# Performance work log

Measured on AMD Instinct MI355X. Metric: run time of the kernel, lower is better.

Reference implementation:

```python
import jax, jax.numpy as jnp
import numpy as np

B = 2097152          # number of query points (e.g. one per pixel of a ~1448^2 image)
N_CTRL = 62          # N_ctrl_pts from __init__
GRID = N_CTRL + 2    # control grid size = 64
MASK_B = 1           # maskBoundary
A = -0.75            # PyTorch bicubic convolution coefficient


def _cubic_weights(t):
    # Weights of the Keys cubic kernel (a=-0.75) for taps at offsets (-1,0,1,2).
    # t in [0,1) is the fractional coordinate. Shapes: t [b] -> [b,4].
    s = 1.0 - t
    w0 = A * t * s * s                      # cc2(t+1)
    w1 = (A + 2.0) * t**3 - (A + 3.0) * t**2 + 1.0   # cc1(t)
    w2 = (A + 2.0) * s**3 - (A + 3.0) * s**2 + 1.0   # cc1(1-t)
    w3 = A * s * t * t                      # cc2(2-t)
    return jnp.stack([w0, w1, w2, w3], axis=-1)


def _reflect(idx, size):
    # PyTorch reflection padding with align_corners=True: reflect about 0 and size-1.
    period = 2 * (size - 1)
    idx = jnp.abs(idx) % period
    return jnp.where(idx >= size, period - idx, idx)


def _bicubic_sample(img, coordinate):
    # img: [c, H, W] (same for every query); coordinate: [b, 2] as (y, x) in [-1,1].
    # Equivalent to: affine_grid(theta, size=(b,c,1,1), align_corners=True) +
    # grid_sample(mode='bicubic', padding_mode='reflection', align_corners=True)
    # where theta = [[1/H, 0, x], [0, 1/H, y]] -> single sample at (x-1/H, y-1/H).
    c, H, W = img.shape
    crop = 1.0 / H
    gx = coordinate[:, 1] - crop   # grid x indexes width
    gy = coordinate[:, 0] - crop   # grid y indexes height
    ix = (gx + 1.0) * 0.5 * (W - 1)   # unnormalize, align_corners=True
    iy = (gy + 1.0) * 0.5 * (H - 1)
    ix0 = jnp.floor(ix)
    iy0 = jnp.floor(iy)
    tx = ix - ix0                      # fractional parts (differentiable wrt coords)
    ty = iy - iy0
    offs = jnp.arange(-1, 3, dtype=jnp.int32)
    xs = jnp.clip(_reflect(ix0.astype(jnp.int32)[:, None] + offs, W), 0, W - 1)  # [b,4]
    ys = jnp.clip(_reflect(iy0.astype(jnp.int32)[:, None] + offs, H), 0, H - 1)  # [b,4]
    wx = _cubic_weights(tx)  # [b,4]
    wy = _cubic_weights(ty)  # [b,4]
    # gather 4x4 neighborhoods: vals[c,b,i,j] = img[c, ys[b,i], xs[b,j]]
    vals = img[:, ys[:, :, None], xs[:, None, :]]  # [c, b, 4, 4]
    return jnp.einsum('cbij,bi,bj->bc', vals, wy, wx)  # [b, c]


def _forward(coordinate, depl_ctr_pts, mask):
    img = depl_ctr_pts * mask          # masked control-point displacement field [2,H,W]
    return _bicubic_sample(img, coordinate)  # [b, 2] (torch.squeeze of [b,2,1,1])


def setup_inputs() -> dict:
    key = jax.random.key(0)
    k1, k2 = jax.random.split(key)
    max_ampl = 1.0 / (N_CTRL - 1)
    depl = (jax.random.uniform(k1, (2, GRID, GRID), jnp.float32) - 0.5) * 2.0 * max_ampl
    border = jnp.zeros((GRID,), bool).at[:MASK_B].set(True).at[-MASK_B:].set(True)
    bm = border[:, None] | border[None, :]
    mask = jnp.where(bm[None, :, :], 0.0, jnp.ones((2, GRID, GRID), jnp.float32))
    depl = depl * mask  # __init__ zeros the boundary ring of the stored param too
    coordinate = jax.random.uniform(k2, (B, 2), jnp.float32, minval=-1.0, maxval=1.0)
    return {"coordinate": coordinate, "depl_ctr_pts": depl, "mask": mask}


def reference(coordinate, depl_ctr_pts, mask):
    return _forward(coordinate, depl_ctr_pts, mask)
```

## Files before the change

### kernel.cpp

```cpp
#include <hip/hip_runtime.h>
#include <hip/hip_fp16.h>

#define TPB 256
#define MAXGRID 2048

#define PW 68

__device__ __forceinline__ void cubic_w(float t, float w[4]) {
    float s = 1.0f - t;
    float t2 = t * t;
    float s2 = s * s;
    w[0] = -0.75f * t * s2;
    w[1] = 1.25f * (t2 * t) - 2.25f * t2 + 1.0f;
    w[2] = 1.25f * (s2 * s) - 2.25f * s2 + 1.0f;
    w[3] = -0.75f * s * t2;
}

__global__ __launch_bounds__(TPB, 8) void deformation_field_kernel(
        const float4* __restrict__ coord4,
        const float4* __restrict__ depl4,
        const float4* __restrict__ mask4,
        float4* __restrict__ out4,
        int n_pairs)
{
    __shared__ __half2 img[PW * PW];

    for (int i = threadIdx.x; i < 1024; i += TPB) {
        float4 d0 = depl4[i];
        float4 m0 = mask4[i];
        float4 d1 = depl4[1024 + i];
        float4 m1 = mask4[1024 + i];
        int o = i * 4;
        int r = o >> 6;
        int c = o & 63;
        int pb = (r + 2) * PW + (c + 2);
        img[pb + 0] = __floats2half2_rn(d0.x * m0.x, d1.x * m1.x);
        img[pb + 1] = __floats2half2_rn(d0.y * m0.y, d1.y * m1.y);
        img[pb + 2] = __floats2half2_rn(d0.z * m0.z, d1.z * m1.z);
        img[pb + 3] = __floats2half2_rn(d0.w * m0.w, d1.w * m1.w);
    }
    __syncthreads();

    {
        int t = threadIdx.x;
        int r = 2 + (t & 63);
        int j = t >> 6;
        int sel = j & 1, half = j >> 1;
        int dc = half ? (66 + sel) : sel;
        int sc = half ? (64 - sel) : (4 - sel);
        img[r * PW + dc] = img[r * PW + sc];
    }
    __syncthreads();

    if (threadIdx.x < PW) {
        int c = threadIdx.x;
        img[0 * PW + c]  = img[4 * PW + c];
        img[1 * PW + c]  = img[3 * PW + c];
        img[66 * PW + c] = img[64 * PW + c];
        img[67 * PW + c] = img[63 * PW + c];
    }
    __syncthreads();

    const int stride = gridDim.x * TPB;
    int p = blockIdx.x * TPB + threadIdx.x;
    if (p >= n_pairs) return;

    float4 c = coord4[p];
    for (;;) {
        int pn = p + stride;
        bool has = (pn < n_pairs);
        float4 cn;
        if (has) cn = coord4[pn];

        float res[4];
        #pragma unroll
        for (int q = 0; q < 2; ++q) {
            float cyv = q ? c.z : c.x;
            float cxv = q ? c.w : c.y;
            float ix = (cxv + 0.984375f) * 31.5f;
            float iy = (cyv + 0.984375f) * 31.5f;
            float fx = floorf(ix);
            float fy = floorf(iy);
            float tx = ix - fx;
            float ty = iy - fy;
            int jx = (int)fx;
            int jy = (int)fy;

            float wx[4], wy[4];
            cubic_w(tx, wx);
            cubic_w(ty, wy);

            int base = (jy + 1) * PW + (jx + 1);

            float a0 = 0.0f, a1 = 0.0f;
            #pragma unroll
            for (int i = 0; i < 4; ++i) {
                int rb = base + i * PW;
                __half2 t0 = img[rb + 0];
                __half2 t1 = img[rb + 1];
                __half2 t2 = img[rb + 2];
                __half2 t3 = img[rb + 3];
                float r0 = wx[0] * __low2float(t0);
                float r1 = wx[0] * __high2float(t0);
                r0 = fmaf(wx[1], __low2float(t1), r0);
                r1 = fmaf(wx[1], __high2float(t1), r1);
                r0 = fmaf(wx[2], __low2float(t2), r0);
                r1 = fmaf(wx[2], __high2float(t2), r1);
                r0 = fmaf(wx[3], __low2float(t3), r0);
                r1 = fmaf(wx[3], __high2float(t3), r1);
                a0 = fmaf(wy[i], r0, a0);
                a1 = fmaf(wy[i], r1, a1);
            }
            res[2 * q + 0] = a0;
            res[2 * q + 1] = a1;
        }
        out4[p] = make_float4(res[0], res[1], res[2], res[3]);

        if (!has) break;
        p = pn;
        c = cn;
    }
}

extern "C" void kernel_launch(void* const* d_in, const int* in_sizes, int n_in,
                              void* d_out, int out_size, void* d_ws, size_t ws_size,
                              hipStream_t stream) {
    const float4* coord4 = (const float4*)d_in[0];
    const float4* depl4  = (const float4*)d_in[1];
    const float4* mask4  = (const float4*)d_in[2];
    float4* out4 = (float4*)d_out;

    int n_pairs = in_sizes[0] / 4;
    int grid = (n_pairs + 2 * TPB - 1) / (2 * TPB);
    if (grid > MAXGRID) grid = MAXGRID;
    if (grid < 1) grid = 1;

    deformation_field_kernel<<<grid, TPB, 0, stream>>>(coord4, depl4, mask4, out4, n_pairs);
}
```

Before: 78.81 us.

## Process one point per thread and do horizontal cubic taps in packed half2

Each thread now handles one query point (float2 loads and stores) instead of a pair, which doubles the work items per grid-stride pass. The horizontal 4-tap filter is computed with packed half2 FMAs on both channels at once, and only the vertical accumulation stays in fp32. This cuts the count of conversion and FMA instructions per sample. The cost is lower accumulation precision in fp16 and narrower 8-byte memory accesses in place of 16-byte ones.

```diff
diff --git a/kernel.cpp b/kernel.cpp
--- a/kernel.cpp
+++ b/kernel.cpp
@@ -17,11 +17,11 @@
 }
 
 __global__ __launch_bounds__(TPB, 8) void deformation_field_kernel(
-        const float4* __restrict__ coord4,
+        const float2* __restrict__ coord2,
         const float4* __restrict__ depl4,
         const float4* __restrict__ mask4,
-        float4* __restrict__ out4,
-        int n_pairs)
+        float2* __restrict__ out2,
+        int n_pts)
 {
     __shared__ __half2 img[PW * PW];
 
@@ -63,58 +63,45 @@
 
     const int stride = gridDim.x * TPB;
     int p = blockIdx.x * TPB + threadIdx.x;
-    if (p >= n_pairs) return;
+    if (p >= n_pts) return;
 
-    float4 c = coord4[p];
+    float2 c = coord2[p];
     for (;;) {
         int pn = p + stride;
-        bool has = (pn < n_pairs);
-        float4 cn;
-        if (has) cn = coord4[pn];
+        bool has = (pn < n_pts);
+        float2 cn;
+        if (has) cn = coord2[pn];
 
-        float res[4];
+        float ix = fmaf(c.y, 31.5f, 31.0078125f);
+        float iy = fmaf(c.x, 31.5f, 31.0078125f);
+        float fx = floorf(ix);
+        float fy = floorf(iy);
+        float tx = ix - fx;
+        float ty = iy - fy;
+        int jx = (int)fx;
+        int jy = (int)fy;
+
+        float wx[4], wy[4];
+        cubic_w(tx, wx);
+        cubic_w(ty, wy);
+        __half2 wxh[4];
         #pragma unroll
-        for (int q = 0; q < 2; ++q) {
-            float cyv = q ? c.z : c.x;
-            float cxv = q ? c.w : c.y;
-            float ix = (cxv + 0.984375f) * 31.5f;
-            float iy = (cyv + 0.984375f) * 31.5f;
-            float fx = floorf(ix);
-            float fy = floorf(iy);
-            float tx = ix - fx;
-            float ty = iy - fy;
-            int jx = (int)fx;
-            int jy = (int)fy;
+        for (int k = 0; k < 4; ++k) wxh[k] = __float2half2_rn(wx[k]);
 
-            float wx[4], wy[4];
-            cubic_w(tx, wx);
-            cubic_w(ty, wy);
+        int base = (jy + 1) * PW + (jx + 1);
 
-            int base = (jy + 1) * PW + (jx + 1);
-
-            float a0 = 0.0f, a1 = 0.0f;
-            #pragma unroll
-            for (int i = 0; i < 4; ++i) {
-                int rb = base + i * PW;
-                __half2 t0 = img[rb + 0];
-                __half2 t1 = img[rb + 1];
-                __half2 t2 = img[rb + 2];
-                __half2 t3 = img[rb + 3];
-                float r0 = wx[0] * __low2float(t0);
-                float r1 = wx[0] * __high2float(t0);
-                r0 = fmaf(wx[1], __low2float(t1), r0);
-                r1 = fmaf(wx[1], __high2float(t1), r1);
-                r0 = fmaf(wx[2], __low2float(t2), r0);
-                r1 = fmaf(wx[2], __high2float(t2), r1);
-                r0 = fmaf(wx[3], __low2float(t3), r0);
-                r1 = fmaf(wx[3], __high2float(t3), r1);
-                a0 = fmaf(wy[i], r0, a0);
-                a1 = fmaf(wy[i], r1, a1);
-            }
-            res[2 * q + 0] = a0;
-            res[2 * q + 1] = a1;
+        float a0 = 0.0f, a1 = 0.0f;
+        #pragma unroll
+        for (int i = 0; i < 4; ++i) {
+            int rb = base + i * PW;
+            __half2 r = __hmul2(wxh[0], img[rb + 0]);
+            r = __hfma2(wxh[1], img[rb + 1], r);
+            r = __hfma2(wxh[2], img[rb + 2], r);
+            r = __hfma2(wxh[3], img[rb + 3], r);
+            a0 = fmaf(wy[i], __low2float(r), a0);
+            a1 = fmaf(wy[i], __high2float(r), a1);
         }
-        out4[p] = make_float4(res[0], res[1], res[2], res[3]);
+        out2[p] = make_float2(a0, a1);
 
         if (!has) break;
         p = pn;
@@ -125,15 +112,15 @@
 extern "C" void kernel_launch(void* const* d_in, const int* in_sizes, int n_in,
                               void* d_out, int out_size, void* d_ws, size_t ws_size,
                               hipStream_t stream) {
-    const float4* coord4 = (const float4*)d_in[0];
+    const float2* coord2 = (const float2*)d_in[0];
     const float4* depl4  = (const float4*)d_in[1];
     const float4* mask4  = (const float4*)d_in[2];
-    float4* out4 = (float4*)d_out;
+    float2* out2 = (float2*)d_out;
 
-    int n_pairs = in_sizes[0] / 4;
-    int grid = (n_pairs + 2 * TPB - 1) / (2 * TPB);
+    int n_pts = in_sizes[0] / 2;
+    int grid = (n_pts + TPB - 1) / TPB;
     if (grid > MAXGRID) grid = MAXGRID;
     if (grid < 1) grid = 1;
 
-    deformation_field_kernel<<<grid, TPB, 0, stream>>>(coord4, depl4, mask4, out4, n_pairs);
+    deformation_field_kernel<<<grid, TPB, 0, stream>>>(coord2, depl4, mask4, out2, n_pts);
 }
```

After: 79.36 us. Within noise of the previous version (+0.7%).
